# Kernel optimization log

Hardware: AMD Instinct MI355X
Metric: run time of the kernel (lower is better)

The kernel has to match this reference:

```python
import jax, jax.numpy as jnp
import numpy as np


def _D(i):
    # discount: 1 / log2(1 + i)
    return 1.0 / jnp.log2(1.0 + i)


def _class_loss(scores_c, mask):
    """NDCG surrogate loss for one class. scores_c: [B] float, mask: [B] bool (concrete)."""
    Ctot = scores_c.shape[0]
    P = int(mask.sum())
    N = Ctot - P
    if P == 0 or N == 0:
        return scores_c.sum() * 0.0
    s_plus = -jnp.sort(-scores_c[mask])       # positives, descending [P]
    s_minus = jnp.sort(scores_c[~mask])       # negatives, ascending  [N] (matches in-place quicksort partitioning)
    Cconst = _D(jnp.arange(1, P + 1, dtype=jnp.float32)).sum()

    # Vectorized equivalent of the recursive calc_optimal_interleaving_rank:
    # opt[m] = argmax_{l in [1, P+1]} sum_{k=l}^{P} -2*(s_plus[k-1]-s_minus[m])/(P*N)
    #                                + (D(l+m) - D(P+m+1))/Cconst
    l = jnp.arange(1, P + 2, dtype=jnp.float32)                       # [P+1]
    # suffix sums of s_plus: Sl[i] = sum_{k=i}^{P-1} s_plus[k], length P+1 (last = 0)
    Sl = jnp.concatenate([jnp.cumsum(s_plus[::-1])[::-1], jnp.zeros(1, s_plus.dtype)])
    cnt = jnp.arange(P, -1, -1, dtype=jnp.float32)                    # P+1-l  [P+1]
    m = jnp.arange(N, dtype=jnp.float32)[:, None]                     # [N,1]
    sm = jax.lax.stop_gradient(s_minus)
    opt_vals = (-2.0 / (P * N)) * (Sl[None, :] - cnt[None, :] * sm[:, None]) \
               + (_D(l[None, :] + m) - _D(float(P) + m + 1.0)) / Cconst   # [N, P+1]
    opt = l[jnp.argmax(opt_vals, axis=1)]                             # [N] float interleaving ranks

    # calc_cs (all constants w.r.t. gradients, as in the torch no_grad blocks)
    i1 = jnp.arange(1, P + 1, dtype=jnp.float32)                      # [P]
    r_plus = 1.0 + jnp.sum(opt[None, :] <= i1[:, None], axis=1)       # [P]
    Delta = 1.0 - _D(jnp.arange(P, dtype=jnp.float32) + r_plus).sum() / Cconst
    c_plus = N + 2.0 - 2.0 * r_plus
    c_minus = P + 2.0 - 2.0 * opt

    F_R = jnp.dot(s_plus, c_plus) + jnp.dot(s_minus, c_minus)
    F_R_star = N * s_plus.sum() - P * s_minus.sum()   # c_plus*=N, c_minus*=-P
    return Delta + (F_R - F_R_star) / (P * N)


def setup_inputs() -> dict:
    key = jax.random.key(0)
    k1, k2 = jax.random.split(key)
    B, n_classes = 16384, 10
    scores = jax.random.normal(k1, (B, n_classes), dtype=jnp.float32)
    labels = jax.random.randint(k2, (B,), 0, n_classes)
    return {"scores": scores, "labels": labels, "n_classes": n_classes}


def reference(scores, labels, n_classes):
    loss = jnp.float32(0.0)
    for c in range(n_classes):
        loss = loss + _class_loss(scores[:, c], labels == c)
    return loss / n_classes
```

## Files before the change

kernel.cpp:

```cpp
#include <hip/hip_runtime.h>
#include <stdint.h>
#include <math.h>

typedef unsigned int u32;
typedef unsigned long long u64;

#define NBUCKET 16384
#define BSHIFT  18
#define HBINS 16512
#define SMAX 2560

__device__ __forceinline__ u32 f2key(float f){
  u32 b = __float_as_uint(f);
  return (b & 0x80000000u) ? ~b : (b | 0x80000000u);
}

__device__ __forceinline__ double blk_reduce_d(double v, int tid, double* ds){
  int lane = tid & 63, wid = tid >> 6;
  for (int off=32; off>0; off>>=1) v += __shfl_down(v, off);
  if (lane==0) ds[wid] = v;
  __syncthreads();
  if (tid < 64){
    double t = (tid<16)? ds[tid] : 0.0;
    for (int off=8; off>0; off>>=1) t += __shfl_down(t, off);
    if (tid==0) ds[16] = t;
  }
  __syncthreads();
  double r = ds[16];
  __syncthreads();
  return r;
}

__device__ __forceinline__ double blk_scan_incl_d(double v, int tid, double* ds){
  int lane = tid & 63, wid = tid >> 6;
  double sv = v;
  for (int off=1; off<64; off<<=1){
    double o = __shfl_up(sv, off);
    if (lane >= off) sv += o;
  }
  if (lane==63) ds[wid] = sv;
  __syncthreads();
  if (tid < 64){
    double w = (tid<16)? ds[tid] : 0.0;
    for (int off=1; off<16; off<<=1){
      double o = __shfl_up(w, off);
      if (tid >= off) w += o;
    }
    if (tid<16) ds[tid] = w;
  }
  __syncthreads();
  double add = (wid>0)? ds[wid-1] : 0.0;
  return sv + add;
}

__device__ __forceinline__ u32 blk_scan_incl_u32(u32 v, int tid, u32* ws){
  int lane = tid & 63, wid = tid >> 6;
  u32 sv = v;
  for (int off=1; off<64; off<<=1){
    u32 o = __shfl_up(sv, off);
    if (lane >= off) sv += o;
  }
  if (lane==63) ws[wid] = sv;
  __syncthreads();
  if (tid < 64){
    u32 w = (tid<16)? ws[tid] : 0u;
    for (int off=1; off<16; off<<=1){
      u32 o = __shfl_up(w, off);
      if (tid >= off) w += o;
    }
    if (tid<16) ws[tid] = w;
  }
  __syncthreads();
  u32 add = (wid>0)? ws[wid-1] : 0u;
  return sv + add;
}

__global__ void k_hist(const float* __restrict__ scores, const int* __restrict__ labels,
                       int B, int NC, u32* __restrict__ bhist,
                       float* __restrict__ Dsh, int SD){
  int t = blockIdx.x*256 + threadIdx.x;
  if (t < 4*SD){
    int p = t / SD, y = t - p*SD;
    long long x = (long long)y + p;
    Dsh[t] = (x==0) ? 0.0f : (float)(1.0/log2(1.0 + (double)x));
  }
  if (t >= B*NC) return;
  int b = t / NC, c = t - (t/NC)*NC;
  float v = scores[t];
  int isPos = (labels[b] == c);
  u32 u = f2key(v);
  u32 bucket = u >> BSHIFT;
  int pi = c*2 + (isPos ? 0 : 1);
  atomicAdd(&bhist[(size_t)pi*NBUCKET + bucket], 1u);
}

__global__ void k_scan(const u32* __restrict__ bhist, u32* __restrict__ bstart,
                       u32* __restrict__ bcursor, u32* __restrict__ Pcnt){
  __shared__ u32 ws[17];
  int pi = blockIdx.x, tid = threadIdx.x;
  const u32* h = bhist + (size_t)pi*NBUCKET;
  u32 v[16]; u32 tot = 0u;
  #pragma unroll
  for (int k=0;k<16;k++){ v[k] = h[tid*16+k]; tot += v[k]; }
  u32 incl = blk_scan_incl_u32(tot, tid, ws);
  u32 run = incl - tot;
  u32* bs = bstart  + (size_t)pi*(NBUCKET+1);
  u32* bc = bcursor + (size_t)pi*NBUCKET;
  #pragma unroll
  for (int k=0;k<16;k++){ bs[tid*16+k]=run; bc[tid*16+k]=run; run+=v[k]; }
  if (tid==1023){
    bs[NBUCKET]=incl;
    if ((pi & 1) == 0) Pcnt[pi >> 1] = incl;
  }
}

__global__ void k_scatter(const float* __restrict__ scores, const int* __restrict__ labels,
                          int B, int NC, u32* __restrict__ bcursor, u64* __restrict__ keyArr){
  int t = blockIdx.x*256 + threadIdx.x;
  if (t >= B*NC) return;
  int b = t / NC, c = t - (t/NC)*NC;
  float v = scores[t];
  int isPos = (labels[b] == c);
  u32 u = f2key(v);
  u32 bucket = u >> BSHIFT;
  int pi = c*2 + (isPos ? 0 : 1);
  u32 slot = atomicAdd(&bcursor[(size_t)pi*NBUCKET + bucket], 1u);
  keyArr[(size_t)pi*B + slot] = ((u64)u << 32) | (u32)b;
}

__global__ void k_rank(const u64* __restrict__ keyArr, const u32* __restrict__ bstart,
                       const u32* __restrict__ Pcnt, int B,
                       float* __restrict__ sPos, float* __restrict__ sNeg){
  int pi = blockIdx.y; int c = pi >> 1; int part = pi & 1;
  u32 P = Pcnt[c];
  u32 cnt = part ? ((u32)B - P) : P;
  u32 t = blockIdx.x*256 + threadIdx.x;
  if (t >= cnt) return;
  const u64* ka = keyArr + (size_t)pi*B;
  u64 K = ka[t];
  u32 bucket = (u32)(K >> (32 + BSHIFT));
  const u32* bs = bstart + (size_t)pi*(NBUCKET+1);
  u32 lo = bs[bucket], hi = bs[bucket+1];
  u32 r = lo;
  for (u32 x=lo; x<hi; ++x) r += (ka[x] < K) ? 1u : 0u;
  u32 u = (u32)(K >> 32);
  u32 bits = (u & 0x80000000u) ? (u & 0x7fffffffu) : ~u;
  float val = __uint_as_float(bits);
  if (part == 0) sPos[(size_t)c*B + (P-1u-r)] = val;
  else           sNeg[(size_t)c*B + r]        = val;
}

__global__ void k_pre(const float* __restrict__ sPos, const u32* __restrict__ Pcnt,
                      const float* __restrict__ Dsh, int B, int strideAB,
                      float* __restrict__ Aarr, float* __restrict__ Barr,
                      double* __restrict__ Cconst){
  __shared__ double ds[17];
  int c = blockIdx.x, tid = threadIdx.x;
  u32 P = Pcnt[c]; u32 N = (u32)B - P;
  if (P==0 || N==0){ if (tid==0) Cconst[c]=1.0; return; }

  double s=0.0;
  for (u32 i=1+tid; i<=P; i+=1024) s += (double)Dsh[i];
  double Cc = blk_reduce_d(s, tid, ds);
  if (tid==0) Cconst[c]=Cc;

  const float* sp = sPos + (size_t)c*B;
  double ts=0.0;
  for (u32 i=tid; i<P; i+=1024) ts += (double)sp[i];
  double totSp = blk_reduce_d(ts, tid, ds);

  double PN = (double)P*(double)N;
  double ca = -2.0*Cc/PN;
  double cb =  2.0*Cc/PN;
  float* A  = Aarr + (size_t)c*strideAB;
  float* Bc = Barr + (size_t)c*strideAB;

  double carry=0.0;
  int nch = ((int)P + 1023)/1024;
  for (int ch=0; ch<nch; ++ch){
    int x = ch*1024 + tid;
    double v = (x < (int)P) ? (double)sp[x] : 0.0;
    double incl = blk_scan_incl_d(v, tid, ds);
    if (x < (int)P){
      double excl = incl - v + carry;
      double Sl = totSp - excl;
      A[x]  = (float)(ca*Sl);
      Bc[x] = (float)(cb*(double)(P-(u32)x));
    }
    carry += ds[15];
    __syncthreads();
  }
  if (tid==0){ A[P]=0.0f; Bc[P]=0.0f; }
}

__global__ void k_main(const float* __restrict__ sNeg, const u32* __restrict__ Pcnt,
                       const float* __restrict__ Dsh, int SD,
                       const float* __restrict__ Aarr, const float* __restrict__ Barr,
                       int B, int strideAB, u64* __restrict__ partKey){
  __shared__ __align__(16) float sA[SMAX];
  __shared__ __align__(16) float sB[SMAX];
  int cy = blockIdx.y;
  int c = cy >> 1, half = cy & 1;
  u32 P = Pcnt[c]; u32 N = (u32)B - P;
  int w    = threadIdx.x >> 6;
  int lane = threadIdx.x & 63;
  int m = blockIdx.x*256 + w + 4*lane;
  const float* A  = Aarr + (size_t)c*strideAB;
  const float* Bc = Barr + (size_t)c*strideAB;
  bool classValid = (P>0u && N>0u);
  int total = (int)P + 1;
  int halfLen = ((total + 7) >> 3) << 2;
  int j0 = half * halfLen;
  int j1 = min(total, j0 + halfLen);
  int len = j1 - j0;
  bool useLds = classValid && (len > 0) && (len <= SMAX - 4);
  if (useLds){
    const float4* A4 = (const float4*)(A + j0);
    const float4* B4 = (const float4*)(Bc + j0);
    float4* sA4 = (float4*)sA;
    float4* sB4 = (float4*)sB;
    int nv = (len + 3) >> 2;
    for (int i = threadIdx.x; i < nv; i += 256){ sA4[i] = A4[i]; sB4[i] = B4[i]; }
  }
  __syncthreads();

  if (classValid && m < (int)N){
    if (len <= 0){
      partKey[(size_t)cy*B + m] = 0ull;
      return;
    }
    float sm = sNeg[(size_t)c*B + m];
    int ph = (m+1) & 3;
    const float* Dp = Dsh + (size_t)ph*SD + (m+1-ph);
    float best = -3.402823466e38f; u32 bj = (u32)j0;
    if (useLds){
      int lenv = len & ~3;
      int i = 0;
      #pragma unroll 2
      for (; i < lenv; i += 4){
        float4 d = *(const float4*)(Dp + j0 + i);
        float4 a = *(const float4*)(sA + i);
        float4 b = *(const float4*)(sB + i);
        float f0 = fmaf(b.x, sm, a.x) + d.x;
        float f1 = fmaf(b.y, sm, a.y) + d.y;
        float f2 = fmaf(b.z, sm, a.z) + d.z;
        float f3 = fmaf(b.w, sm, a.w) + d.w;
        if (f0 > best){ best=f0; bj=(u32)(j0+i); }
        if (f1 > best){ best=f1; bj=(u32)(j0+i+1); }
        if (f2 > best){ best=f2; bj=(u32)(j0+i+2); }
        if (f3 > best){ best=f3; bj=(u32)(j0+i+3); }
      }
      for (; i < len; ++i){
        float f = fmaf(sB[i], sm, sA[i]) + Dp[j0+i];
        if (f > best){ best=f; bj=(u32)(j0+i); }
      }
    } else {
      int jv = j0 + (len & ~3);
      int j = j0;
      #pragma unroll 2
      for (; j < jv; j += 4){
        float4 d = *(const float4*)(Dp + j);
        float4 a = *(const float4*)(A + j);
        float4 b = *(const float4*)(Bc + j);
        float f0 = fmaf(b.x, sm, a.x) + d.x;
        float f1 = fmaf(b.y, sm, a.y) + d.y;
        float f2 = fmaf(b.z, sm, a.z) + d.z;
        float f3 = fmaf(b.w, sm, a.w) + d.w;
        if (f0 > best){ best=f0; bj=(u32)j; }
        if (f1 > best){ best=f1; bj=(u32)(j+1); }
        if (f2 > best){ best=f2; bj=(u32)(j+2); }
        if (f3 > best){ best=f3; bj=(u32)(j+3); }
      }
      for (; j < j1; ++j){
        float f = fmaf(Bc[j], sm, A[j]) + Dp[j];
        if (f > best){ best=f; bj=(u32)j; }
      }
    }
    partKey[(size_t)cy*B + m] = ((u64)f2key(best + 0.0f) << 32) | (u32)(~bj);
  }
}

__global__ void k_finish(const float* __restrict__ sPos, const float* __restrict__ sNeg,
                         const u32* __restrict__ Pcnt,
                         const u64* __restrict__ partKey, const float* __restrict__ Dsh,
                         const double* __restrict__ Cconst,
                         int B, int NC,
                         u64* __restrict__ classLoss, u32* __restrict__ doneCount,
                         float* __restrict__ out){
  __shared__ u32 hbins[HBINS];
  __shared__ u32 ws[17];
  __shared__ double ds[17];
  int c = blockIdx.x, tid = threadIdx.x;
  u32 P = Pcnt[c]; u32 N = (u32)B - P;
  double myLoss = 0.0;
  if (P!=0 && N!=0){
    const u64* pk0 = partKey + (size_t)(c*2+0)*B;
    const u64* pk1 = partKey + (size_t)(c*2+1)*B;
    const float* sp = sPos + (size_t)c*B;
    const float* sn = sNeg + (size_t)c*B;
    double sumD=0.0, sumSpr=0.0, sumSp=0.0, S1=0.0, S2=0.0;
    if ((int)P + 2 <= HBINS){
      for (int i = tid; i < (int)P + 2; i += 1024) hbins[i] = 0u;
      __syncthreads();
      for (int m2 = tid; m2 < (int)N; m2 += 1024){
        u64 k0 = pk0[m2], k1 = pk1[m2];
        u64 kk = (k0 > k1) ? k0 : k1;
        u32 opt = (~(u32)kk) + 1u;
        atomicAdd(&hbins[opt], 1u);
        double smv = (double)sn[m2];
        S1 += smv;
        S2 += smv * (double)opt;
      }
      __syncthreads();
      u32 carry=0u;
      int nch = ((int)P + 1023)/1024;
      for (int ch=0; ch<nch; ++ch){
        int x = ch*1024 + tid;
        u32 v = (x < (int)P) ? hbins[x+1] : 0u;
        u32 incl = blk_scan_incl_u32(v, tid, ws);
        u32 cum = incl + carry;
        if (x < (int)P){
          u32 r = 1u + cum;
          float spv = sp[x];
          sumD   += (double)Dsh[x + r];
          sumSpr += (double)spv * (double)r;
          sumSp  += (double)spv;
        }
        carry += ws[15];
        __syncthreads();
      }
    } else {
      for (int m2 = tid; m2 < (int)N; m2 += 1024){
        u64 k0 = pk0[m2], k1 = pk1[m2];
        u64 kk = (k0 > k1) ? k0 : k1;
        u32 opt = (~(u32)kk) + 1u;
        double smv = (double)sn[m2];
        S1 += smv; S2 += smv * (double)opt;
      }
      for (int x = tid; x < (int)P; x += 1024){
        u32 target = (u32)x + 1u, cnt2 = 0u;
        for (u32 m2 = 0; m2 < N; ++m2){
          u64 k0 = pk0[m2], k1 = pk1[m2];
          u64 kk = (k0 > k1) ? k0 : k1;
          u32 opt = (~(u32)kk) + 1u;
          cnt2 += (opt <= target) ? 1u : 0u;
        }
        u32 r = 1u + cnt2;
        float spv = sp[x];
        sumD   += (double)Dsh[x + r];
        sumSpr += (double)spv * (double)r;
        sumSp  += (double)spv;
      }
    }
    double totD   = blk_reduce_d(sumD,   tid, ds);
    double totSpr = blk_reduce_d(sumSpr, tid, ds);
    double totSp  = blk_reduce_d(sumSp,  tid, ds);
    double S1t    = blk_reduce_d(S1,     tid, ds);
    double S2t    = blk_reduce_d(S2,     tid, ds);
    if (tid==0){
      double Cc = Cconst[c];
      double Delta = 1.0 - totD/Cc;
      double Fp    = (double)(N+2u)*totSp - 2.0*totSpr;
      double Fm    = (double)(P+2u)*S1t  - 2.0*S2t;
      double Fstar = (double)N*totSp - (double)P*S1t;
      myLoss = Delta + (Fp + Fm - Fstar)/((double)P*(double)N);
    }
  }
  if (tid==0){
    atomicExch(&classLoss[c], (u64)__double_as_longlong(myLoss));
    __threadfence();
    u32 old = atomicAdd(doneCount, 1u);
    if (old == (u32)gridDim.x - 1u){
      __threadfence();
      double s=0.0;
      for (int cc=0; cc<NC; ++cc){
        u64 bits = atomicAdd(&classLoss[cc], 0ull);
        s += __longlong_as_double((long long)bits);
      }
      out[0] = (float)(s/(double)NC);
    }
  }
}

extern "C" void kernel_launch(void* const* d_in, const int* in_sizes, int n_in,
                              void* d_out, int out_size, void* d_ws, size_t ws_size,
                              hipStream_t stream) {
  const float* scores = (const float*)d_in[0];
  const int*   labels = (const int*)d_in[1];
  int B  = in_sizes[1];
  int NC = in_sizes[0] / in_sizes[1];
  float* out = (float*)d_out;

  int SD = B + 8;
  int strideAB = B + 8;
  int nblkM = (B + 255)/256;

  char* ws = (char*)d_ws;
  size_t off = 0;
  auto alloc = [&](size_t bytes)->char* {
    char* p = ws + off;
    off = (off + bytes + 255) & ~(size_t)255;
    return p;
  };
  float* Dsh = (float*)alloc((size_t)4*SD*4);
  char* zbeg = ws + off;
  u32* bhist     = (u32*)alloc((size_t)NC*2*NBUCKET*4);
  u32* doneCount = (u32*)alloc(4);
  char* zend = ws + off;
  u32* Pcnt      = (u32*)alloc((size_t)NC*4);
  u32* bstart    = (u32*)alloc((size_t)NC*2*(NBUCKET+1)*4);
  u32* bcursor   = (u32*)alloc((size_t)NC*2*NBUCKET*4);
  u64* keyArr    = (u64*)alloc((size_t)NC*2*B*8);
  float* sPos    = (float*)alloc((size_t)NC*B*4);
  float* sNeg    = (float*)alloc((size_t)NC*B*4);
  float* Aarr    = (float*)alloc((size_t)NC*strideAB*4);
  float* Barr    = (float*)alloc((size_t)NC*strideAB*4);
  double* Cconst = (double*)alloc((size_t)NC*8);
  u64* partKey   = (u64*)alloc((size_t)NC*2*B*8);
  u64* classLoss = (u64*)alloc((size_t)NC*8);

  hipMemsetAsync(zbeg, 0, (size_t)(zend - zbeg), stream);

  k_hist<<<(B*NC+255)/256, 256, 0, stream>>>(scores, labels, B, NC, bhist, Dsh, SD);
  k_scan<<<NC*2, 1024, 0, stream>>>(bhist, bstart, bcursor, Pcnt);
  k_scatter<<<(B*NC+255)/256, 256, 0, stream>>>(scores, labels, B, NC, bcursor, keyArr);
  k_rank<<<dim3((B+255)/256, NC*2), 256, 0, stream>>>(keyArr, bstart, Pcnt, B, sPos, sNeg);
  k_pre<<<NC, 1024, 0, stream>>>(sPos, Pcnt, Dsh, B, strideAB, Aarr, Barr, Cconst);
  k_main<<<dim3(nblkM, NC*2), 256, 0, stream>>>(sNeg, Pcnt, Dsh, SD, Aarr, Barr,
                                                B, strideAB, partKey);
  k_finish<<<NC, 1024, 0, stream>>>(sPos, sNeg, Pcnt, partKey, Dsh, Cconst, B, NC,
                                    classLoss, doneCount, out);
}
```

Baseline: 168.0 us.

## Process two negatives per thread and use group-max argmax with deferred index recovery

After: 165.2 us. About the same (-1.7%).

```diff
diff --git a/kernel.cpp b/kernel.cpp
--- a/kernel.cpp
+++ b/kernel.cpp
@@ -204,7 +204,8 @@
   u32 P = Pcnt[c]; u32 N = (u32)B - P;
   int w    = threadIdx.x >> 6;
   int lane = threadIdx.x & 63;
-  int m = blockIdx.x*256 + w + 4*lane;
+  int m0 = blockIdx.x*512 + w + 4*lane;
+  int m1 = m0 + 256;
   const float* A  = Aarr + (size_t)c*strideAB;
   const float* Bc = Barr + (size_t)c*strideAB;
   bool classValid = (P>0u && N>0u);
@@ -224,59 +225,124 @@
   }
   __syncthreads();
 
-  if (classValid && m < (int)N){
+  bool v0 = classValid && (m0 < (int)N);
+  bool v1 = classValid && (m1 < (int)N);
+  if (v0){
     if (len <= 0){
-      partKey[(size_t)cy*B + m] = 0ull;
+      partKey[(size_t)cy*B + m0] = 0ull;
+      if (v1) partKey[(size_t)cy*B + m1] = 0ull;
       return;
     }
-    float sm = sNeg[(size_t)c*B + m];
-    int ph = (m+1) & 3;
-    const float* Dp = Dsh + (size_t)ph*SD + (m+1-ph);
-    float best = -3.402823466e38f; u32 bj = (u32)j0;
+    float sm0 = sNeg[(size_t)c*B + m0];
+    float sm1 = v1 ? sNeg[(size_t)c*B + m1] : 0.0f;
+    int ph = (m0+1) & 3;
+    const float* Dp0 = Dsh + (size_t)ph*SD + (m0+1-ph);
+    const float* Dp1 = v1 ? (Dp0 + 256) : Dp0;
+    float best0 = -3.402823466e38f, best1 = -3.402823466e38f;
+    u32 bj0 = (u32)j0, bj1 = (u32)j0;
+    int bg0 = -1, bg1 = -1;
     if (useLds){
       int lenv = len & ~3;
       int i = 0;
       #pragma unroll 2
       for (; i < lenv; i += 4){
-        float4 d = *(const float4*)(Dp + j0 + i);
         float4 a = *(const float4*)(sA + i);
         float4 b = *(const float4*)(sB + i);
-        float f0 = fmaf(b.x, sm, a.x) + d.x;
-        float f1 = fmaf(b.y, sm, a.y) + d.y;
-        float f2 = fmaf(b.z, sm, a.z) + d.z;
-        float f3 = fmaf(b.w, sm, a.w) + d.w;
-        if (f0 > best){ best=f0; bj=(u32)(j0+i); }
-        if (f1 > best){ best=f1; bj=(u32)(j0+i+1); }
-        if (f2 > best){ best=f2; bj=(u32)(j0+i+2); }
-        if (f3 > best){ best=f3; bj=(u32)(j0+i+3); }
+        float4 d0 = *(const float4*)(Dp0 + j0 + i);
+        float4 d1 = *(const float4*)(Dp1 + j0 + i);
+        float p0 = fmaf(b.x, sm0, a.x) + d0.x;
+        float p1 = fmaf(b.y, sm0, a.y) + d0.y;
+        float p2 = fmaf(b.z, sm0, a.z) + d0.z;
+        float p3 = fmaf(b.w, sm0, a.w) + d0.w;
+        float q0 = fmaf(b.x, sm1, a.x) + d1.x;
+        float q1 = fmaf(b.y, sm1, a.y) + d1.y;
+        float q2 = fmaf(b.z, sm1, a.z) + d1.z;
+        float q3 = fmaf(b.w, sm1, a.w) + d1.w;
+        float g0 = fmaxf(fmaxf(p0,p1), fmaxf(p2,p3));
+        float g1 = fmaxf(fmaxf(q0,q1), fmaxf(q2,q3));
+        if (g0 > best0){ best0 = g0; bg0 = j0 + i; }
+        if (g1 > best1){ best1 = g1; bg1 = j0 + i; }
       }
       for (; i < len; ++i){
-        float f = fmaf(sB[i], sm, sA[i]) + Dp[j0+i];
-        if (f > best){ best=f; bj=(u32)(j0+i); }
+        float f0 = fmaf(sB[i], sm0, sA[i]) + Dp0[j0+i];
+        float f1 = fmaf(sB[i], sm1, sA[i]) + Dp1[j0+i];
+        if (f0 > best0){ best0=f0; bj0=(u32)(j0+i); bg0 = -2; }
+        if (f1 > best1){ best1=f1; bj1=(u32)(j0+i); bg1 = -2; }
+      }
+      if (bg0 >= 0){
+        int i2 = bg0 - j0;
+        float4 a = *(const float4*)(sA + i2);
+        float4 b = *(const float4*)(sB + i2);
+        float4 d = *(const float4*)(Dp0 + bg0);
+        float f0 = fmaf(b.x, sm0, a.x) + d.x;
+        float f1 = fmaf(b.y, sm0, a.y) + d.y;
+        float f2 = fmaf(b.z, sm0, a.z) + d.z;
+        u32 o = (f0==best0) ? 0u : (f1==best0) ? 1u : (f2==best0) ? 2u : 3u;
+        bj0 = (u32)bg0 + o;
+      }
+      if (bg1 >= 0){
+        int i2 = bg1 - j0;
+        float4 a = *(const float4*)(sA + i2);
+        float4 b = *(const float4*)(sB + i2);
+        float4 d = *(const float4*)(Dp1 + bg1);
+        float f0 = fmaf(b.x, sm1, a.x) + d.x;
+        float f1 = fmaf(b.y, sm1, a.y) + d.y;
+        float f2 = fmaf(b.z, sm1, a.z) + d.z;
+        u32 o = (f0==best1) ? 0u : (f1==best1) ? 1u : (f2==best1) ? 2u : 3u;
+        bj1 = (u32)bg1 + o;
       }
     } else {
       int jv = j0 + (len & ~3);
       int j = j0;
       #pragma unroll 2
       for (; j < jv; j += 4){
-        float4 d = *(const float4*)(Dp + j);
         float4 a = *(const float4*)(A + j);
         float4 b = *(const float4*)(Bc + j);
-        float f0 = fmaf(b.x, sm, a.x) + d.x;
-        float f1 = fmaf(b.y, sm, a.y) + d.y;
-        float f2 = fmaf(b.z, sm, a.z) + d.z;
-        float f3 = fmaf(b.w, sm, a.w) + d.w;
-        if (f0 > best){ best=f0; bj=(u32)j; }
-        if (f1 > best){ best=f1; bj=(u32)(j+1); }
-        if (f2 > best){ best=f2; bj=(u32)(j+2); }
-        if (f3 > best){ best=f3; bj=(u32)(j+3); }
+        float4 d0 = *(const float4*)(Dp0 + j);
+        float4 d1 = *(const float4*)(Dp1 + j);
+        float p0 = fmaf(b.x, sm0, a.x) + d0.x;
+        float p1 = fmaf(b.y, sm0, a.y) + d0.y;
+        float p2 = fmaf(b.z, sm0, a.z) + d0.z;
+        float p3 = fmaf(b.w, sm0, a.w) + d0.w;
+        float q0 = fmaf(b.x, sm1, a.x) + d1.x;
+        float q1 = fmaf(b.y, sm1, a.y) + d1.y;
+        float q2 = fmaf(b.z, sm1, a.z) + d1.z;
+        float q3 = fmaf(b.w, sm1, a.w) + d1.w;
+        float g0 = fmaxf(fmaxf(p0,p1), fmaxf(p2,p3));
+        float g1 = fmaxf(fmaxf(q0,q1), fmaxf(q2,q3));
+        if (g0 > best0){ best0 = g0; bg0 = j; }
+        if (g1 > best1){ best1 = g1; bg1 = j; }
       }
       for (; j < j1; ++j){
-        float f = fmaf(Bc[j], sm, A[j]) + Dp[j];
-        if (f > best){ best=f; bj=(u32)j; }
-      }
-    }
-    partKey[(size_t)cy*B + m] = ((u64)f2key(best + 0.0f) << 32) | (u32)(~bj);
+        float f0 = fmaf(Bc[j], sm0, A[j]) + Dp0[j];
+        float f1 = fmaf(Bc[j], sm1, A[j]) + Dp1[j];
+        if (f0 > best0){ best0=f0; bj0=(u32)j; bg0 = -2; }
+        if (f1 > best1){ best1=f1; bj1=(u32)j; bg1 = -2; }
+      }
+      if (bg0 >= 0){
+        float4 a = *(const float4*)(A + bg0);
+        float4 b = *(const float4*)(Bc + bg0);
+        float4 d = *(const float4*)(Dp0 + bg0);
+        float f0 = fmaf(b.x, sm0, a.x) + d.x;
+        float f1 = fmaf(b.y, sm0, a.y) + d.y;
+        float f2 = fmaf(b.z, sm0, a.z) + d.z;
+        u32 o = (f0==best0) ? 0u : (f1==best0) ? 1u : (f2==best0) ? 2u : 3u;
+        bj0 = (u32)bg0 + o;
+      }
+      if (bg1 >= 0){
+        float4 a = *(const float4*)(A + bg1);
+        float4 b = *(const float4*)(Bc + bg1);
+        float4 d = *(const float4*)(Dp1 + bg1);
+        float f0 = fmaf(b.x, sm1, a.x) + d.x;
+        float f1 = fmaf(b.y, sm1, a.y) + d.y;
+        float f2 = fmaf(b.z, sm1, a.z) + d.z;
+        u32 o = (f0==best1) ? 0u : (f1==best1) ? 1u : (f2==best1) ? 2u : 3u;
+        bj1 = (u32)bg1 + o;
+      }
+    }
+    partKey[(size_t)cy*B + m0] = ((u64)f2key(best0 + 0.0f) << 32) | (u32)(~bj0);
+    if (v1)
+      partKey[(size_t)cy*B + m1] = ((u64)f2key(best1 + 0.0f) << 32) | (u32)(~bj1);
   }
 }
 
@@ -393,7 +459,7 @@
 
   int SD = B + 8;
   int strideAB = B + 8;
-  int nblkM = (B + 255)/256;
+  int nblkM = (B + 511)/512;
 
   char* ws = (char*)d_ws;
   size_t off = 0;
```
